# Kernel optimization log

Measured on AMD Instinct MI355X. Metric: run time of the kernel, lower is better.

Reference implementation:

```python
import jax, jax.numpy as jnp
import numpy as np

DIM = 1024
HEADS = 16
HEAD_DIM = DIM // HEADS
HIDDEN = 4 * DIM
B, N = 4, 2048


def _layernorm(x, g, b, eps=1e-5):
    mu = jnp.mean(x, axis=-1, keepdims=True)
    var = jnp.var(x, axis=-1, keepdims=True)
    return (x - mu) * jax.lax.rsqrt(var + eps) * g + b


def setup_inputs() -> dict:
    key = jax.random.key(0)
    ks = jax.random.split(key, 8)
    s_in = 1.0 / np.sqrt(DIM)
    s_hid = 1.0 / np.sqrt(HIDDEN)
    return {
        "x": jax.random.normal(ks[0], (B, N, DIM), jnp.float32),
        "w_qkv": jax.random.normal(ks[1], (DIM, 3 * DIM), jnp.float32) * s_in,
        "w_proj": jax.random.normal(ks[2], (DIM, DIM), jnp.float32) * s_in,
        "b_proj": jnp.zeros((DIM,), jnp.float32),
        "ln1_g": jnp.ones((DIM,), jnp.float32),
        "ln1_b": jnp.zeros((DIM,), jnp.float32),
        "w1": jax.random.normal(ks[3], (DIM, HIDDEN), jnp.float32) * s_in,
        "b1": jnp.zeros((HIDDEN,), jnp.float32),
        "w2": jax.random.normal(ks[4], (HIDDEN, DIM), jnp.float32) * s_hid,
        "b2": jnp.zeros((DIM,), jnp.float32),
        "ln2_g": jnp.ones((DIM,), jnp.float32),
        "ln2_b": jnp.zeros((DIM,), jnp.float32),
    }


def reference(x, w_qkv, w_proj, b_proj, ln1_g, ln1_b, w1, b1, w2, b2, ln2_g, ln2_b):
    # --- multi-head self-attention (pre-norm), dropout=0 (eval) ---
    h = _layernorm(x, ln1_g, ln1_b)
    qkv = h @ w_qkv                       # [B,N,3*DIM]
    qkv = qkv.reshape(B, N, 3, HEADS, HEAD_DIM)
    q = jnp.transpose(qkv[:, :, 0], (0, 2, 1, 3))  # [B,H,N,hd]
    k = jnp.transpose(qkv[:, :, 1], (0, 2, 1, 3))
    v = jnp.transpose(qkv[:, :, 2], (0, 2, 1, 3))
    scale = HEAD_DIM ** -0.5
    attn = jnp.einsum('bhqd,bhkd->bhqk', q, k) * scale  # [B,H,N,N]
    attn = jax.nn.softmax(attn, axis=-1)
    o = jnp.einsum('bhqk,bhkd->bhqd', attn, v)
    o = jnp.transpose(o, (0, 2, 1, 3)).reshape(B, N, DIM)
    x = o @ w_proj + b_proj + x
    # --- feed-forward (pre-norm), exact GELU ---
    h = _layernorm(x, ln2_g, ln2_b)
    h = jax.nn.gelu(h @ w1 + b1, approximate=False)
    return h @ w2 + b2 + x
```

## Files before the change

kernel.cpp:

```cpp
#include <hip/hip_runtime.h>
#include <cstdint>
#include <cstddef>

typedef float  v4f  __attribute__((ext_vector_type(4)));
typedef __bf16 v8bf __attribute__((ext_vector_type(8)));
typedef __bf16 v4bf __attribute__((ext_vector_type(4)));

__device__ __forceinline__ float b2f(unsigned short u) {
  union { unsigned int i; float f; } cv; cv.i = ((unsigned int)u) << 16; return cv.f;
}
__device__ __forceinline__ unsigned short f2b(float f) {
  union { float f; unsigned int i; } cv; cv.f = f;
  unsigned int i = cv.i;
  i += 0x7fffu + ((i >> 16) & 1u);
  return (unsigned short)(i >> 16);
}
__device__ __forceinline__ unsigned short f2b_trunc(float f) {
  union { float f; unsigned int i; } cv; cv.f = f;
  return (unsigned short)(cv.i >> 16);
}
__device__ __forceinline__ float gelu_fast(float x) {
  const float u = x * (1.5957691216f + 0.07135481627f * x * x);
  return x * (1.0f / (1.0f + __expf(-u)));
}
__device__ __forceinline__ void g2l16(const unsigned short* g, unsigned short* l) {
  __builtin_amdgcn_global_load_lds(
      (const __attribute__((address_space(1))) void*)g,
      (__attribute__((address_space(3))) void*)l,
      16, 0, 0);
}

__global__ __launch_bounds__(256) void transpose_k(const float* __restrict__ in,
                                                   unsigned short* __restrict__ out,
                                                   int R, int C) {
  __shared__ float tile[32][33];
  const int tx = threadIdx.x, ty = threadIdx.y;
  const int r0 = blockIdx.y * 32, c0 = blockIdx.x * 32;
#pragma unroll
  for (int j = 0; j < 4; ++j)
    tile[ty + 8 * j][tx] = in[(size_t)(r0 + ty + 8 * j) * C + c0 + tx];
  __syncthreads();
#pragma unroll
  for (int j = 0; j < 4; ++j)
    out[(size_t)(c0 + ty + 8 * j) * R + r0 + tx] = f2b(tile[tx][ty + 8 * j]);
}

__global__ __launch_bounds__(256) void ln_kernel(const void* __restrict__ xp, int in_bf16,
                                                 const float* __restrict__ g,
                                                 const float* __restrict__ bta,
                                                 unsigned short* __restrict__ out) {
  const int r = blockIdx.x, t = threadIdx.x;
  float v0, v1, v2, v3;
  if (in_bf16) {
    const ushort4 raw = *(const ushort4*)((const unsigned short*)xp + (size_t)r * 1024 + t * 4);
    v0 = b2f(raw.x); v1 = b2f(raw.y); v2 = b2f(raw.z); v3 = b2f(raw.w);
  } else {
    const float4 raw = *(const float4*)((const float*)xp + (size_t)r * 1024 + t * 4);
    v0 = raw.x; v1 = raw.y; v2 = raw.z; v3 = raw.w;
  }
  float s  = v0 + v1 + v2 + v3;
  float s2 = v0 * v0 + v1 * v1 + v2 * v2 + v3 * v3;
#pragma unroll
  for (int off = 32; off > 0; off >>= 1) {
    s  += __shfl_down(s, off);
    s2 += __shfl_down(s2, off);
  }
  __shared__ float red[8];
  const int w = t >> 6, lane = t & 63;
  if (lane == 0) { red[w] = s; red[4 + w] = s2; }
  __syncthreads();
  if (t == 0) {
    float ts = red[0] + red[1] + red[2] + red[3];
    float t2 = red[4] + red[5] + red[6] + red[7];
    float mu = ts * (1.0f / 1024.0f);
    float var = t2 * (1.0f / 1024.0f) - mu * mu;
    red[0] = mu;
    red[1] = rsqrtf(var + 1e-5f);
  }
  __syncthreads();
  const float mu = red[0], rs = red[1];
  const float4 graw = *(const float4*)(g + t * 4);
  const float4 braw = *(const float4*)(bta + t * 4);
  ushort4 o;
  o.x = f2b((v0 - mu) * rs * graw.x + braw.x);
  o.y = f2b((v1 - mu) * rs * graw.y + braw.y);
  o.z = f2b((v2 - mu) * rs * graw.z + braw.z);
  o.w = f2b((v3 - mu) * rs * graw.w + braw.w);
  *(ushort4*)(out + (size_t)r * 1024 + t * 4) = o;
}

__global__ __launch_bounds__(256, 2) void gemm_bt(const unsigned short* __restrict__ A,
                                                  const unsigned short* __restrict__ Bt,
                                                  const float* __restrict__ bias,
                                                  const void* __restrict__ res, int res_bf16,
                                                  void* __restrict__ Cout,
                                                  int M, int N, int K, int act, int out_bf16,
                                                  int swap_xy) {
  __shared__ __align__(16) unsigned short As[3][128 * 32];
  __shared__ __align__(16) unsigned short Bs[3][128 * 32];
  const int t = threadIdx.x;
  const int lane = t & 63, w = t >> 6;
  const int wr = (w >> 1) * 64, wc = (w & 1) * 64;
  const int lr = lane & 15, lq = lane >> 4;
  const int mb = swap_xy ? blockIdx.x : blockIdx.y;
  const int nb = swap_xy ? blockIdx.y : blockIdx.x;
  const int m0 = mb * 128, n0 = nb * 128;

  const int c0 = t, c1 = t + 256;
  const int r0 = c0 >> 2, o0 = (c0 & 3) << 3;
  const int r1 = c1 >> 2, o1 = (c1 & 3) << 3;
  const unsigned short* Ag0 = A  + (size_t)(m0 + r0) * K + o0;
  const unsigned short* Ag1 = A  + (size_t)(m0 + r1) * K + o1;
  const unsigned short* Bg0 = Bt + (size_t)(n0 + r0) * K + o0;
  const unsigned short* Bg1 = Bt + (size_t)(n0 + r1) * K + o1;

  v4f acc[4][4];
#pragma unroll
  for (int mi = 0; mi < 4; ++mi)
#pragma unroll
    for (int ni = 0; ni < 4; ++ni)
      acc[mi][ni] = (v4f){0.f, 0.f, 0.f, 0.f};

  const int nt = K >> 5;
  g2l16(Ag0, &As[0][c0 * 8]); g2l16(Bg0, &Bs[0][c0 * 8]);
  g2l16(Ag1, &As[0][c1 * 8]); g2l16(Bg1, &Bs[0][c1 * 8]);
  if (nt > 1) {
    g2l16(Ag0 + 32, &As[1][c0 * 8]); g2l16(Bg0 + 32, &Bs[1][c0 * 8]);
    g2l16(Ag1 + 32, &As[1][c1 * 8]); g2l16(Bg1 + 32, &Bs[1][c1 * 8]);
  }

  int bi = 0;
  for (int tt = 0; tt < nt; ++tt) {
    const int pf = tt + 2;
    if (pf < nt) {
      const int ko = pf << 5;
      const int pb = pf % 3;
      g2l16(Ag0 + ko, &As[pb][c0 * 8]); g2l16(Bg0 + ko, &Bs[pb][c0 * 8]);
      g2l16(Ag1 + ko, &As[pb][c1 * 8]); g2l16(Bg1 + ko, &Bs[pb][c1 * 8]);
      asm volatile("s_waitcnt vmcnt(8)" ::: "memory");
    } else if (tt + 1 < nt) {
      asm volatile("s_waitcnt vmcnt(4)" ::: "memory");
    } else {
      asm volatile("s_waitcnt vmcnt(0)" ::: "memory");
    }
    __builtin_amdgcn_s_barrier();
    asm volatile("" ::: "memory");

    v8bf af[4], bfr[4];
#pragma unroll
    for (int i = 0; i < 4; ++i) {
      af[i]  = *(const v8bf*)(&As[bi][(wr + i * 16 + lr) * 32 + lq * 8]);
      bfr[i] = *(const v8bf*)(&Bs[bi][(wc + i * 16 + lr) * 32 + lq * 8]);
    }
#pragma unroll
    for (int mi = 0; mi < 4; ++mi)
#pragma unroll
      for (int ni = 0; ni < 4; ++ni)
        acc[mi][ni] = __builtin_amdgcn_mfma_f32_16x16x32_bf16(af[mi], bfr[ni], acc[mi][ni], 0, 0, 0);

    asm volatile("" ::: "memory");
    __builtin_amdgcn_s_barrier();
    bi = (bi == 2) ? 0 : bi + 1;
  }

#pragma unroll
  for (int mi = 0; mi < 4; ++mi) {
#pragma unroll
    for (int ni = 0; ni < 4; ++ni) {
      const int col = n0 + wc + ni * 16 + lr;
      const float bv = bias ? bias[col] : 0.0f;
#pragma unroll
      for (int r = 0; r < 4; ++r) {
        const int row = m0 + wr + mi * 16 + lq * 4 + r;
        float v = acc[mi][ni][r] + bv;
        if (act) v = gelu_fast(v);
        if (res) {
          v += res_bf16 ? b2f(((const unsigned short*)res)[(size_t)row * N + col])
                        : ((const float*)res)[(size_t)row * N + col];
        }
        if (out_bf16)
          ((unsigned short*)Cout)[(size_t)row * N + col] = f2b(v);
        else
          ((float*)Cout)[(size_t)row * N + col] = v;
      }
    }
  }
}

__global__ __launch_bounds__(256) void vt_k(const unsigned short* __restrict__ qkv,
                                            unsigned short* __restrict__ Vt) {
  const int t = threadIdx.x;
  const int n = blockIdx.x * 256 + t, h = blockIdx.y, b = blockIdx.z;
  const size_t src = (size_t)(b * 2048 + n) * 3072 + 2048 + h * 64;
  unsigned short v[64];
#pragma unroll
  for (int j = 0; j < 8; ++j)
    *(uint4*)(v + j * 8) = *(const uint4*)(qkv + src + j * 8);
  const size_t dstbase = ((size_t)(b * 16 + h) * 64) * 2048 + n;
#pragma unroll
  for (int d = 0; d < 64; ++d)
    Vt[dstbase + (size_t)d * 2048] = v[d];
}

__global__ __launch_bounds__(256, 2) void attn_mfma(const unsigned short* __restrict__ qkv,
                                                    const unsigned short* __restrict__ Vt,
                                                    unsigned short* __restrict__ out) {
  __shared__ __align__(16) unsigned short Ks[64 * 80];
  __shared__ __align__(16) unsigned short Vs[64 * 80];
  __shared__ __align__(16) unsigned short Ps[4][32 * 76];
  const int t = threadIdx.x;
  const int lane = t & 63, w = t >> 6;
  const int lr = lane & 15, lq = lane >> 4;
  const int h = blockIdx.x, b = blockIdx.z;
  const int q0 = blockIdx.y * 128 + w * 32;

  v8bf aq[2][2];
#pragma unroll
  for (int mi = 0; mi < 2; ++mi)
#pragma unroll
    for (int kq = 0; kq < 2; ++kq)
      aq[mi][kq] = *(const v8bf*)(qkv + (size_t)(b * 2048 + q0 + mi * 16 + lr) * 3072
                                  + h * 64 + kq * 32 + lq * 8);

  v4f acc_o[2][4];
  float lsum[2][4];
#pragma unroll
  for (int mi = 0; mi < 2; ++mi)
#pragma unroll
    for (int di = 0; di < 4; ++di)
      acc_o[mi][di] = (v4f){0.f, 0.f, 0.f, 0.f};
#pragma unroll
  for (int mi = 0; mi < 2; ++mi)
#pragma unroll
    for (int r = 0; r < 4; ++r)
      lsum[mi][r] = 0.0f;

  const int sc0 = t, sc1 = t + 256;
  const int kr0 = sc0 >> 3, ko0 = (sc0 & 7) * 8;
  const int kr1 = sc1 >> 3, ko1 = (sc1 & 7) * 8;
  const unsigned short* Kg0 = qkv + (size_t)(b * 2048 + kr0) * 3072 + 1024 + h * 64 + ko0;
  const unsigned short* Kg1 = qkv + (size_t)(b * 2048 + kr1) * 3072 + 1024 + h * 64 + ko1;
  const unsigned short* Vg0 = Vt + ((size_t)(b * 16 + h) * 64 + kr0) * 2048 + ko0;
  const unsigned short* Vg1 = Vt + ((size_t)(b * 16 + h) * 64 + kr1) * 2048 + ko1;

  uint4 kreg0 = *(const uint4*)(Kg0);
  uint4 kreg1 = *(const uint4*)(Kg1);
  uint4 vreg0 = *(const uint4*)(Vg0);
  uint4 vreg1 = *(const uint4*)(Vg1);
  *(uint4*)(Ks + kr0 * 80 + ko0) = kreg0;
  *(uint4*)(Ks + kr1 * 80 + ko1) = kreg1;
  *(uint4*)(Vs + kr0 * 80 + ko0) = vreg0;
  *(uint4*)(Vs + kr1 * 80 + ko1) = vreg1;
  __syncthreads();

  for (int kt = 0; kt < 32; ++kt) {
    if (kt < 31) {
      const size_t kn = (size_t)(kt + 1) * 64;
      kreg0 = *(const uint4*)(Kg0 + kn * 3072);
      kreg1 = *(const uint4*)(Kg1 + kn * 3072);
      vreg0 = *(const uint4*)(Vg0 + kn);
      vreg1 = *(const uint4*)(Vg1 + kn);
    }

    v4f s_acc[2][4];
#pragma unroll
    for (int mi = 0; mi < 2; ++mi)
#pragma unroll
      for (int ni = 0; ni < 4; ++ni)
        s_acc[mi][ni] = (v4f){0.f, 0.f, 0.f, 0.f};
#pragma unroll
    for (int kq = 0; kq < 2; ++kq) {
      v8bf bk[4];
#pragma unroll
      for (int ni = 0; ni < 4; ++ni)
        bk[ni] = *(const v8bf*)(Ks + (ni * 16 + lr) * 80 + kq * 32 + lq * 8);
      __builtin_amdgcn_s_setprio(1);
#pragma unroll
      for (int mi = 0; mi < 2; ++mi)
#pragma unroll
        for (int ni = 0; ni < 4; ++ni)
          s_acc[mi][ni] = __builtin_amdgcn_mfma_f32_16x16x32_bf16(aq[mi][kq], bk[ni], s_acc[mi][ni], 0, 0, 0);
      __builtin_amdgcn_s_setprio(0);
    }

#pragma unroll
    for (int mi = 0; mi < 2; ++mi)
#pragma unroll
      for (int ni = 0; ni < 4; ++ni)
#pragma unroll
        for (int r = 0; r < 4; ++r) {
          const float p = __expf(s_acc[mi][ni][r] * 0.125f);
          const unsigned short pb = f2b_trunc(p);
          lsum[mi][r] += b2f(pb);
          Ps[w][(mi * 16 + lq * 4 + r) * 76 + ni * 16 + lr] = pb;
        }

#pragma unroll
    for (int ks = 0; ks < 2; ++ks) {
      v8bf ap[2], bv[4];
#pragma unroll
      for (int mi = 0; mi < 2; ++mi) {
        const unsigned short* base = Ps[w] + (mi * 16 + lr) * 76 + ks * 32 + lq * 8;
        const v4bf lo = *(const v4bf*)(base);
        const v4bf hi = *(const v4bf*)(base + 4);
        ap[mi] = __builtin_shufflevector(lo, hi, 0, 1, 2, 3, 4, 5, 6, 7);
      }
#pragma unroll
      for (int di = 0; di < 4; ++di)
        bv[di] = *(const v8bf*)(Vs + (di * 16 + lr) * 80 + ks * 32 + lq * 8);
      __builtin_amdgcn_s_setprio(1);
#pragma unroll
      for (int mi = 0; mi < 2; ++mi)
#pragma unroll
        for (int di = 0; di < 4; ++di)
          acc_o[mi][di] = __builtin_amdgcn_mfma_f32_16x16x32_bf16(ap[mi], bv[di], acc_o[mi][di], 0, 0, 0);
      __builtin_amdgcn_s_setprio(0);
    }

    __syncthreads();
    if (kt < 31) {
      *(uint4*)(Ks + kr0 * 80 + ko0) = kreg0;
      *(uint4*)(Ks + kr1 * 80 + ko1) = kreg1;
      *(uint4*)(Vs + kr0 * 80 + ko0) = vreg0;
      *(uint4*)(Vs + kr1 * 80 + ko1) = vreg1;
    }
    __syncthreads();
  }

#pragma unroll
  for (int mi = 0; mi < 2; ++mi)
#pragma unroll
    for (int r = 0; r < 4; ++r) {
      float v = lsum[mi][r];
      v += __shfl_xor(v, 1);
      v += __shfl_xor(v, 2);
      v += __shfl_xor(v, 4);
      v += __shfl_xor(v, 8);
      lsum[mi][r] = 1.0f / v;
    }

#pragma unroll
  for (int mi = 0; mi < 2; ++mi)
#pragma unroll
    for (int di = 0; di < 4; ++di)
#pragma unroll
      for (int r = 0; r < 4; ++r)
        out[(size_t)(b * 2048 + q0 + mi * 16 + lq * 4 + r) * 1024 + h * 64 + di * 16 + lr] =
            f2b(acc_o[mi][di][r] * lsum[mi][r]);
}

extern "C" void kernel_launch(void* const* d_in, const int* in_sizes, int n_in,
                              void* d_out, int out_size, void* d_ws, size_t ws_size,
                              hipStream_t stream) {
  (void)in_sizes; (void)n_in; (void)out_size; (void)ws_size;
  const float* x      = (const float*)d_in[0];
  const float* w_qkv  = (const float*)d_in[1];
  const float* w_proj = (const float*)d_in[2];
  const float* b_proj = (const float*)d_in[3];
  const float* ln1_g  = (const float*)d_in[4];
  const float* ln1_b  = (const float*)d_in[5];
  const float* w1     = (const float*)d_in[6];
  const float* b1     = (const float*)d_in[7];
  const float* w2     = (const float*)d_in[8];
  const float* b2     = (const float*)d_in[9];
  const float* ln2_g  = (const float*)d_in[10];
  const float* ln2_b  = (const float*)d_in[11];
  float* out = (float*)d_out;

  char* ws = (char*)d_ws;
  unsigned short* T_a   = (unsigned short*)(ws);
  unsigned short* T_b   = (unsigned short*)(ws + 8388608);
  unsigned short* x2buf = (unsigned short*)(ws + 16777216);
  unsigned short* Vtbuf = (unsigned short*)(ws + 33554432);
  unsigned short* Hbuf  = (unsigned short*)(ws + 50331648);
  unsigned short* qkvb  = (unsigned short*)(ws + 67108864);
  unsigned short* h3buf = (unsigned short*)(ws + 50331648);
  unsigned short* h2buf = (unsigned short*)d_out;

  const dim3 tb(32, 8);
  transpose_k<<<dim3(96, 32),  tb, 0, stream>>>(w_qkv,  T_a, 1024, 3072);
  transpose_k<<<dim3(32, 32),  tb, 0, stream>>>(w_proj, T_b, 1024, 1024);
  ln_kernel<<<8192, 256, 0, stream>>>(x, 0, ln1_g, ln1_b, Hbuf);
  gemm_bt<<<dim3(24, 64), 256, 0, stream>>>(Hbuf, T_a, nullptr, nullptr, 0, qkvb, 8192, 3072, 1024, 0, 1, 0);
  transpose_k<<<dim3(128, 32), tb, 0, stream>>>(w1, T_a, 1024, 4096);
  vt_k<<<dim3(8, 16, 4), 256, 0, stream>>>(qkvb, Vtbuf);
  attn_mfma<<<dim3(16, 16, 4), 256, 0, stream>>>(qkvb, Vtbuf, Hbuf);
  gemm_bt<<<dim3(64, 8), 256, 0, stream>>>(Hbuf, T_b, b_proj, x, 0, x2buf, 8192, 1024, 1024, 0, 1, 1);
  transpose_k<<<dim3(32, 128), tb, 0, stream>>>(w2, T_b, 4096, 1024);
  ln_kernel<<<8192, 256, 0, stream>>>(x2buf, 1, ln2_g, ln2_b, h2buf);
  gemm_bt<<<dim3(32, 64), 256, 0, stream>>>(h2buf, T_a, b1, nullptr, 0, h3buf, 8192, 4096, 1024, 1, 1, 0);
  gemm_bt<<<dim3(64, 8), 256, 0, stream>>>(h3buf, T_b, b2, x2buf, 1, out, 8192, 1024, 4096, 0, 0, 1);
}
```

Baseline: 583.7 us.

## Swizzle GEMM LDS layout and load attention K/V directly from global

The GEMM kernel now XOR-swizzles the column chunk used for global-to-LDS staging, and the MFMA fragment reads use the matching swizzled offset. This is meant to reduce LDS bank conflicts. The attention kernel drops its shared K/V tiles and block-wide barriers: each wave reads its K and V fragments straight from global memory (relying on cache reuse across waves), and the occupancy hint is raised to 4 blocks. This removes synchronization and LDS traffic, but every wave now issues redundant global loads and no longer prefetches the next tile, so it may expose memory latency.

```diff
diff --git a/kernel.cpp b/kernel.cpp
--- a/kernel.cpp
+++ b/kernel.cpp
@@ -107,12 +107,14 @@
   const int m0 = mb * 128, n0 = nb * 128;
 
   const int c0 = t, c1 = t + 256;
-  const int r0 = c0 >> 2, o0 = (c0 & 3) << 3;
-  const int r1 = c1 >> 2, o1 = (c1 & 3) << 3;
+  const int r0 = c0 >> 2, o0 = (((c0 & 3) ^ ((c0 >> 3) & 3)) << 3);
+  const int r1 = c1 >> 2, o1 = (((c1 & 3) ^ ((c1 >> 3) & 3)) << 3);
   const unsigned short* Ag0 = A  + (size_t)(m0 + r0) * K + o0;
   const unsigned short* Ag1 = A  + (size_t)(m0 + r1) * K + o1;
   const unsigned short* Bg0 = Bt + (size_t)(n0 + r0) * K + o0;
   const unsigned short* Bg1 = Bt + (size_t)(n0 + r1) * K + o1;
+
+  const int ra = ((lq ^ ((lr >> 1) & 3)) << 3);
 
   v4f acc[4][4];
 #pragma unroll
@@ -149,8 +151,8 @@
     v8bf af[4], bfr[4];
 #pragma unroll
     for (int i = 0; i < 4; ++i) {
-      af[i]  = *(const v8bf*)(&As[bi][(wr + i * 16 + lr) * 32 + lq * 8]);
-      bfr[i] = *(const v8bf*)(&Bs[bi][(wc + i * 16 + lr) * 32 + lq * 8]);
+      af[i]  = *(const v8bf*)(&As[bi][(wr + i * 16 + lr) * 32 + ra]);
+      bfr[i] = *(const v8bf*)(&Bs[bi][(wc + i * 16 + lr) * 32 + ra]);
     }
 #pragma unroll
     for (int mi = 0; mi < 4; ++mi)
@@ -202,11 +204,9 @@
     Vt[dstbase + (size_t)d * 2048] = v[d];
 }
 
-__global__ __launch_bounds__(256, 2) void attn_mfma(const unsigned short* __restrict__ qkv,
+__global__ __launch_bounds__(256, 4) void attn_mfma(const unsigned short* __restrict__ qkv,
                                                     const unsigned short* __restrict__ Vt,
                                                     unsigned short* __restrict__ out) {
-  __shared__ __align__(16) unsigned short Ks[64 * 80];
-  __shared__ __align__(16) unsigned short Vs[64 * 80];
   __shared__ __align__(16) unsigned short Ps[4][32 * 76];
   const int t = threadIdx.x;
   const int lane = t & 63, w = t >> 6;
@@ -235,32 +235,11 @@
     for (int r = 0; r < 4; ++r)
       lsum[mi][r] = 0.0f;
 
-  const int sc0 = t, sc1 = t + 256;
-  const int kr0 = sc0 >> 3, ko0 = (sc0 & 7) * 8;
-  const int kr1 = sc1 >> 3, ko1 = (sc1 & 7) * 8;
-  const unsigned short* Kg0 = qkv + (size_t)(b * 2048 + kr0) * 3072 + 1024 + h * 64 + ko0;
-  const unsigned short* Kg1 = qkv + (size_t)(b * 2048 + kr1) * 3072 + 1024 + h * 64 + ko1;
-  const unsigned short* Vg0 = Vt + ((size_t)(b * 16 + h) * 64 + kr0) * 2048 + ko0;
-  const unsigned short* Vg1 = Vt + ((size_t)(b * 16 + h) * 64 + kr1) * 2048 + ko1;
-
-  uint4 kreg0 = *(const uint4*)(Kg0);
-  uint4 kreg1 = *(const uint4*)(Kg1);
-  uint4 vreg0 = *(const uint4*)(Vg0);
-  uint4 vreg1 = *(const uint4*)(Vg1);
-  *(uint4*)(Ks + kr0 * 80 + ko0) = kreg0;
-  *(uint4*)(Ks + kr1 * 80 + ko1) = kreg1;
-  *(uint4*)(Vs + kr0 * 80 + ko0) = vreg0;
-  *(uint4*)(Vs + kr1 * 80 + ko1) = vreg1;
-  __syncthreads();
+  const unsigned short* Kb = qkv + (size_t)b * 2048 * 3072 + 1024 + h * 64 + lq * 8;
+  const unsigned short* Vb = Vt + ((size_t)(b * 16 + h) * 64 + lr) * 2048 + lq * 8;
 
   for (int kt = 0; kt < 32; ++kt) {
-    if (kt < 31) {
-      const size_t kn = (size_t)(kt + 1) * 64;
-      kreg0 = *(const uint4*)(Kg0 + kn * 3072);
-      kreg1 = *(const uint4*)(Kg1 + kn * 3072);
-      vreg0 = *(const uint4*)(Vg0 + kn);
-      vreg1 = *(const uint4*)(Vg1 + kn);
-    }
+    const int kt0 = kt * 64;
 
     v4f s_acc[2][4];
 #pragma unroll
@@ -273,7 +252,7 @@
       v8bf bk[4];
 #pragma unroll
       for (int ni = 0; ni < 4; ++ni)
-        bk[ni] = *(const v8bf*)(Ks + (ni * 16 + lr) * 80 + kq * 32 + lq * 8);
+        bk[ni] = *(const v8bf*)(Kb + (size_t)(kt0 + ni * 16 + lr) * 3072 + kq * 32);
       __builtin_amdgcn_s_setprio(1);
 #pragma unroll
       for (int mi = 0; mi < 2; ++mi)
@@ -282,6 +261,13 @@
           s_acc[mi][ni] = __builtin_amdgcn_mfma_f32_16x16x32_bf16(aq[mi][kq], bk[ni], s_acc[mi][ni], 0, 0, 0);
       __builtin_amdgcn_s_setprio(0);
     }
+
+    v8bf bv[2][4];
+#pragma unroll
+    for (int ks = 0; ks < 2; ++ks)
+#pragma unroll
+      for (int di = 0; di < 4; ++di)
+        bv[ks][di] = *(const v8bf*)(Vb + (size_t)(di * 16) * 2048 + kt0 + ks * 32);
 
 #pragma unroll
     for (int mi = 0; mi < 2; ++mi)
@@ -297,7 +283,7 @@
 
 #pragma unroll
     for (int ks = 0; ks < 2; ++ks) {
-      v8bf ap[2], bv[4];
+      v8bf ap[2];
 #pragma unroll
       for (int mi = 0; mi < 2; ++mi) {
         const unsigned short* base = Ps[w] + (mi * 16 + lr) * 76 + ks * 32 + lq * 8;
@@ -305,26 +291,14 @@
         const v4bf hi = *(const v4bf*)(base + 4);
         ap[mi] = __builtin_shufflevector(lo, hi, 0, 1, 2, 3, 4, 5, 6, 7);
       }
-#pragma unroll
-      for (int di = 0; di < 4; ++di)
-        bv[di] = *(const v8bf*)(Vs + (di * 16 + lr) * 80 + ks * 32 + lq * 8);
       __builtin_amdgcn_s_setprio(1);
 #pragma unroll
       for (int mi = 0; mi < 2; ++mi)
 #pragma unroll
         for (int di = 0; di < 4; ++di)
-          acc_o[mi][di] = __builtin_amdgcn_mfma_f32_16x16x32_bf16(ap[mi], bv[di], acc_o[mi][di], 0, 0, 0);
+          acc_o[mi][di] = __builtin_amdgcn_mfma_f32_16x16x32_bf16(ap[mi], bv[ks][di], acc_o[mi][di], 0, 0, 0);
       __builtin_amdgcn_s_setprio(0);
     }
-
-    __syncthreads();
-    if (kt < 31) {
-      *(uint4*)(Ks + kr0 * 80 + ko0) = kreg0;
-      *(uint4*)(Ks + kr1 * 80 + ko1) = kreg1;
-      *(uint4*)(Vs + kr0 * 80 + ko0) = vreg0;
-      *(uint4*)(Vs + kr1 * 80 + ko1) = vreg1;
-    }
-    __syncthreads();
   }
 
 #pragma unroll
```

Result: slower. 751.8 us (+28.8%).

## Enlarge GEMM tile to 256x128 with XOR-swizzled LDS layout

Applied to the files above, without the earlier changes.

The GEMM block tile grows from 128x128 to 256x128, with each wave computing a 128x64 output (8x4 MFMA tiles), and all GEMM launch grids are halved in M to match. The LDS chunk offsets are XOR-swizzled on both the global-to-LDS store and the fragment reads to reduce bank conflicts. This raises arithmetic intensity per B-tile load and cuts the number of blocks. In exchange it doubles the accumulator registers and uses more LDS (about 72 KB), which may lower occupancy below the launch bound. It also leaves fewer blocks for the N=1024 GEMMs (256 blocks).

```diff
diff --git a/kernel.cpp b/kernel.cpp
--- a/kernel.cpp
+++ b/kernel.cpp
@@ -96,75 +96,91 @@
                                                   void* __restrict__ Cout,
                                                   int M, int N, int K, int act, int out_bf16,
                                                   int swap_xy) {
-  __shared__ __align__(16) unsigned short As[3][128 * 32];
+  __shared__ __align__(16) unsigned short As[3][256 * 32];
   __shared__ __align__(16) unsigned short Bs[3][128 * 32];
   const int t = threadIdx.x;
   const int lane = t & 63, w = t >> 6;
-  const int wr = (w >> 1) * 64, wc = (w & 1) * 64;
+  const int wr = (w >> 1) * 128, wc = (w & 1) * 64;
   const int lr = lane & 15, lq = lane >> 4;
   const int mb = swap_xy ? blockIdx.x : blockIdx.y;
   const int nb = swap_xy ? blockIdx.y : blockIdx.x;
-  const int m0 = mb * 128, n0 = nb * 128;
-
-  const int c0 = t, c1 = t + 256;
-  const int r0 = c0 >> 2, o0 = (c0 & 3) << 3;
-  const int r1 = c1 >> 2, o1 = (c1 & 3) << 3;
-  const unsigned short* Ag0 = A  + (size_t)(m0 + r0) * K + o0;
-  const unsigned short* Ag1 = A  + (size_t)(m0 + r1) * K + o1;
-  const unsigned short* Bg0 = Bt + (size_t)(n0 + r0) * K + o0;
-  const unsigned short* Bg1 = Bt + (size_t)(n0 + r1) * K + o1;
-
-  v4f acc[4][4];
-#pragma unroll
-  for (int mi = 0; mi < 4; ++mi)
+  const int m0 = mb * 256, n0 = nb * 128;
+
+  const unsigned short* Ag0;
+  const unsigned short* Ag1;
+  const unsigned short* Ag2;
+  const unsigned short* Ag3;
+  const unsigned short* Bg0;
+  const unsigned short* Bg1;
+  {
+    const int cA0 = t,        rA0 = cA0 >> 2, oA0 = (((cA0 & 3) ^ ((cA0 >> 3) & 3)) << 3);
+    const int cA1 = t + 256,  rA1 = cA1 >> 2, oA1 = (((cA1 & 3) ^ ((cA1 >> 3) & 3)) << 3);
+    const int cA2 = t + 512,  rA2 = cA2 >> 2, oA2 = (((cA2 & 3) ^ ((cA2 >> 3) & 3)) << 3);
+    const int cA3 = t + 768,  rA3 = cA3 >> 2, oA3 = (((cA3 & 3) ^ ((cA3 >> 3) & 3)) << 3);
+    Ag0 = A + (size_t)(m0 + rA0) * K + oA0;
+    Ag1 = A + (size_t)(m0 + rA1) * K + oA1;
+    Ag2 = A + (size_t)(m0 + rA2) * K + oA2;
+    Ag3 = A + (size_t)(m0 + rA3) * K + oA3;
+    Bg0 = Bt + (size_t)(n0 + rA0) * K + oA0;
+    Bg1 = Bt + (size_t)(n0 + rA1) * K + oA1;
+  }
+  const int ra = ((lq ^ ((lr >> 1) & 3)) << 3);
+
+  v4f acc[8][4];
+#pragma unroll
+  for (int mi = 0; mi < 8; ++mi)
 #pragma unroll
     for (int ni = 0; ni < 4; ++ni)
       acc[mi][ni] = (v4f){0.f, 0.f, 0.f, 0.f};
 
+#define STAGE(buf, ko)                                  \
+  do {                                                  \
+    g2l16(Ag0 + (ko), &As[buf][(t)*8]);                 \
+    g2l16(Ag1 + (ko), &As[buf][(t + 256) * 8]);         \
+    g2l16(Ag2 + (ko), &As[buf][(t + 512) * 8]);         \
+    g2l16(Ag3 + (ko), &As[buf][(t + 768) * 8]);         \
+    g2l16(Bg0 + (ko), &Bs[buf][(t)*8]);                 \
+    g2l16(Bg1 + (ko), &Bs[buf][(t + 256) * 8]);         \
+  } while (0)
+
   const int nt = K >> 5;
-  g2l16(Ag0, &As[0][c0 * 8]); g2l16(Bg0, &Bs[0][c0 * 8]);
-  g2l16(Ag1, &As[0][c1 * 8]); g2l16(Bg1, &Bs[0][c1 * 8]);
-  if (nt > 1) {
-    g2l16(Ag0 + 32, &As[1][c0 * 8]); g2l16(Bg0 + 32, &Bs[1][c0 * 8]);
-    g2l16(Ag1 + 32, &As[1][c1 * 8]); g2l16(Bg1 + 32, &Bs[1][c1 * 8]);
-  }
+  STAGE(0, 0);
+  STAGE(1, 32);
 
   int bi = 0;
   for (int tt = 0; tt < nt; ++tt) {
     const int pf = tt + 2;
     if (pf < nt) {
-      const int ko = pf << 5;
-      const int pb = pf % 3;
-      g2l16(Ag0 + ko, &As[pb][c0 * 8]); g2l16(Bg0 + ko, &Bs[pb][c0 * 8]);
-      g2l16(Ag1 + ko, &As[pb][c1 * 8]); g2l16(Bg1 + ko, &Bs[pb][c1 * 8]);
-      asm volatile("s_waitcnt vmcnt(8)" ::: "memory");
+      STAGE(pf % 3, pf << 5);
+      asm volatile("s_waitcnt vmcnt(12)" ::: "memory");
     } else if (tt + 1 < nt) {
-      asm volatile("s_waitcnt vmcnt(4)" ::: "memory");
+      asm volatile("s_waitcnt vmcnt(6)" ::: "memory");
     } else {
       asm volatile("s_waitcnt vmcnt(0)" ::: "memory");
     }
     __builtin_amdgcn_s_barrier();
     asm volatile("" ::: "memory");
 
-    v8bf af[4], bfr[4];
-#pragma unroll
-    for (int i = 0; i < 4; ++i) {
-      af[i]  = *(const v8bf*)(&As[bi][(wr + i * 16 + lr) * 32 + lq * 8]);
-      bfr[i] = *(const v8bf*)(&Bs[bi][(wc + i * 16 + lr) * 32 + lq * 8]);
-    }
-#pragma unroll
-    for (int mi = 0; mi < 4; ++mi)
+    v8bf bfr[4];
+#pragma unroll
+    for (int i = 0; i < 4; ++i)
+      bfr[i] = *(const v8bf*)(&Bs[bi][(wc + i * 16 + lr) * 32 + ra]);
+#pragma unroll
+    for (int mi = 0; mi < 8; ++mi) {
+      const v8bf af = *(const v8bf*)(&As[bi][(wr + mi * 16 + lr) * 32 + ra]);
 #pragma unroll
       for (int ni = 0; ni < 4; ++ni)
-        acc[mi][ni] = __builtin_amdgcn_mfma_f32_16x16x32_bf16(af[mi], bfr[ni], acc[mi][ni], 0, 0, 0);
+        acc[mi][ni] = __builtin_amdgcn_mfma_f32_16x16x32_bf16(af, bfr[ni], acc[mi][ni], 0, 0, 0);
+    }
 
     asm volatile("" ::: "memory");
     __builtin_amdgcn_s_barrier();
     bi = (bi == 2) ? 0 : bi + 1;
   }
-
-#pragma unroll
-  for (int mi = 0; mi < 4; ++mi) {
+#undef STAGE
+
+#pragma unroll
+  for (int mi = 0; mi < 8; ++mi) {
 #pragma unroll
     for (int ni = 0; ni < 4; ++ni) {
       const int col = n0 + wc + ni * 16 + lr;
@@ -313,7 +329,7 @@
       for (int mi = 0; mi < 2; ++mi)
 #pragma unroll
         for (int di = 0; di < 4; ++di)
-          acc_o[mi][di] = __builtin_amdgcn_mfma_f32_16x16x32_bf16(ap[mi], bv[di], acc_o[mi][di], 0, 0, 0);
+          acc_o[mi][di] = __builtin_amdgcn_mfma_f32_16x16x32_bf16(ap[mi], bv[ks == 0 ? di : di], acc_o[mi][di], 0, 0, 0);
       __builtin_amdgcn_s_setprio(0);
     }
 
@@ -381,13 +397,13 @@
   transpose_k<<<dim3(96, 32),  tb, 0, stream>>>(w_qkv,  T_a, 1024, 3072);
   transpose_k<<<dim3(32, 32),  tb, 0, stream>>>(w_proj, T_b, 1024, 1024);
   ln_kernel<<<8192, 256, 0, stream>>>(x, 0, ln1_g, ln1_b, Hbuf);
-  gemm_bt<<<dim3(24, 64), 256, 0, stream>>>(Hbuf, T_a, nullptr, nullptr, 0, qkvb, 8192, 3072, 1024, 0, 1, 0);
+  gemm_bt<<<dim3(24, 32), 256, 0, stream>>>(Hbuf, T_a, nullptr, nullptr, 0, qkvb, 8192, 3072, 1024, 0, 1, 0);
   transpose_k<<<dim3(128, 32), tb, 0, stream>>>(w1, T_a, 1024, 4096);
   vt_k<<<dim3(8, 16, 4), 256, 0, stream>>>(qkvb, Vtbuf);
   attn_mfma<<<dim3(16, 16, 4), 256, 0, stream>>>(qkvb, Vtbuf, Hbuf);
-  gemm_bt<<<dim3(64, 8), 256, 0, stream>>>(Hbuf, T_b, b_proj, x, 0, x2buf, 8192, 1024, 1024, 0, 1, 1);
+  gemm_bt<<<dim3(32, 8), 256, 0, stream>>>(Hbuf, T_b, b_proj, x, 0, x2buf, 8192, 1024, 1024, 0, 1, 1);
   transpose_k<<<dim3(32, 128), tb, 0, stream>>>(w2, T_b, 4096, 1024);
   ln_kernel<<<8192, 256, 0, stream>>>(x2buf, 1, ln2_g, ln2_b, h2buf);
-  gemm_bt<<<dim3(32, 64), 256, 0, stream>>>(h2buf, T_a, b1, nullptr, 0, h3buf, 8192, 4096, 1024, 1, 1, 0);
-  gemm_bt<<<dim3(64, 8), 256, 0, stream>>>(h3buf, T_b, b2, x2buf, 1, out, 8192, 1024, 4096, 0, 0, 1);
-}
+  gemm_bt<<<dim3(32, 32), 256, 0, stream>>>(h2buf, T_a, b1, nullptr, 0, h3buf, 8192, 4096, 1024, 1, 1, 0);
+  gemm_bt<<<dim3(32, 8), 256, 0, stream>>>(h3buf, T_b, b2, x2buf, 1, out, 8192, 1024, 4096, 0, 0, 1);
+}
```

After: 672.4 us. 1.15x slower.

## Replace GEMM with 8-wave 256xBN tile kernel using swizzled LDS and phased MFMA

Applied to the files above, without the earlier changes.

Replaces the 128x128 four-wave GEMM with a templated eight-wave kernel that uses 256x256 or 256x128 output tiles, a K-step of 64, and double-buffered LDS. The LDS layout gets an XOR swizzle to avoid bank conflicts. The MFMA work is split into quadrant phases, with barriers and s_setprio, so the A and B stage-ins are interleaved with compute. The goal is more data reuse per block and better overlap of global loads with MFMA. In exchange it uses more registers and LDS per block, and fewer blocks on the projection and FFN2 GEMMs (256 blocks) may leave CUs underfilled.

```diff
diff --git a/kernel.cpp b/kernel.cpp
--- a/kernel.cpp
+++ b/kernel.cpp
@@ -89,84 +89,177 @@
   *(ushort4*)(out + (size_t)r * 1024 + t * 4) = o;
 }
 
-__global__ __launch_bounds__(256, 2) void gemm_bt(const unsigned short* __restrict__ A,
-                                                  const unsigned short* __restrict__ Bt,
-                                                  const float* __restrict__ bias,
-                                                  const void* __restrict__ res, int res_bf16,
-                                                  void* __restrict__ Cout,
-                                                  int M, int N, int K, int act, int out_bf16,
-                                                  int swap_xy) {
-  __shared__ __align__(16) unsigned short As[3][128 * 32];
-  __shared__ __align__(16) unsigned short Bs[3][128 * 32];
+template <int NREP>
+__global__ __launch_bounds__(512, 2) void gemm8p(const unsigned short* __restrict__ A,
+                                                 const unsigned short* __restrict__ Bt,
+                                                 const float* __restrict__ bias,
+                                                 const void* __restrict__ res, int res_bf16,
+                                                 void* __restrict__ Cout,
+                                                 int M, int N, int K, int act, int out_bf16,
+                                                 int swap_xy) {
+  constexpr int BN = NREP * 64;
+  __shared__ __align__(16) unsigned short As[2][256 * 64];
+  __shared__ __align__(16) unsigned short Bs[2][BN * 64];
   const int t = threadIdx.x;
-  const int lane = t & 63, w = t >> 6;
-  const int wr = (w >> 1) * 64, wc = (w & 1) * 64;
+  const int lane = t & 63;
   const int lr = lane & 15, lq = lane >> 4;
+  const int wid = t >> 6;
+  const int wm = wid >> 2, wn = wid & 3;
   const int mb = swap_xy ? blockIdx.x : blockIdx.y;
   const int nb = swap_xy ? blockIdx.y : blockIdx.x;
-  const int m0 = mb * 128, n0 = nb * 128;
-
-  const int c0 = t, c1 = t + 256;
-  const int r0 = c0 >> 2, o0 = (c0 & 3) << 3;
-  const int r1 = c1 >> 2, o1 = (c1 & 3) << 3;
-  const unsigned short* Ag0 = A  + (size_t)(m0 + r0) * K + o0;
-  const unsigned short* Ag1 = A  + (size_t)(m0 + r1) * K + o1;
-  const unsigned short* Bg0 = Bt + (size_t)(n0 + r0) * K + o0;
-  const unsigned short* Bg1 = Bt + (size_t)(n0 + r1) * K + o1;
-
-  v4f acc[4][4];
-#pragma unroll
-  for (int mi = 0; mi < 4; ++mi)
-#pragma unroll
-    for (int ni = 0; ni < 4; ++ni)
+  const int m0 = mb * 256, n0 = nb * BN;
+
+  const int srow = t >> 3;
+  const int schunk = (t & 7) ^ (srow & 7);
+  const unsigned short* Agp[4];
+  const unsigned short* Bgp[NREP];
+#pragma unroll
+  for (int j = 0; j < 4; ++j)
+    Agp[j] = A + (size_t)(m0 + j * 64 + srow) * K + schunk * 8;
+#pragma unroll
+  for (int j = 0; j < NREP; ++j)
+    Bgp[j] = Bt + (size_t)(n0 + j * 64 + srow) * K + schunk * 8;
+
+  auto stageA = [&](int dbuf, int ko) {
+#pragma unroll
+    for (int j = 0; j < 4; ++j)
+      g2l16(Agp[j] + ko, &As[dbuf][j * 4096 + t * 8]);
+  };
+  auto stageB = [&](int dbuf, int ko) {
+#pragma unroll
+    for (int j = 0; j < NREP; ++j)
+      g2l16(Bgp[j] + ko, &Bs[dbuf][j * 4096 + t * 8]);
+  };
+  auto lda = [&](int dbuf, int mi, int kq) -> v8bf {
+    return *(const v8bf*)(&As[dbuf][(wm * 128 + mi * 16 + lr) * 64 +
+                                    (((kq * 4 + lq) ^ (lr & 7)) << 3)]);
+  };
+  auto ldb = [&](int dbuf, int ni, int kq) -> v8bf {
+    return *(const v8bf*)(&Bs[dbuf][(wn * (BN / 4) + ni * 16 + lr) * 64 +
+                                    (((kq * 4 + lq) ^ (lr & 7)) << 3)]);
+  };
+
+  v4f acc[8][NREP];
+#pragma unroll
+  for (int mi = 0; mi < 8; ++mi)
+#pragma unroll
+    for (int ni = 0; ni < NREP; ++ni)
       acc[mi][ni] = (v4f){0.f, 0.f, 0.f, 0.f};
 
-  const int nt = K >> 5;
-  g2l16(Ag0, &As[0][c0 * 8]); g2l16(Bg0, &Bs[0][c0 * 8]);
-  g2l16(Ag1, &As[0][c1 * 8]); g2l16(Bg1, &Bs[0][c1 * 8]);
-  if (nt > 1) {
-    g2l16(Ag0 + 32, &As[1][c0 * 8]); g2l16(Bg0 + 32, &Bs[1][c0 * 8]);
-    g2l16(Ag1 + 32, &As[1][c1 * 8]); g2l16(Bg1 + 32, &Bs[1][c1 * 8]);
-  }
-
-  int bi = 0;
-  for (int tt = 0; tt < nt; ++tt) {
-    const int pf = tt + 2;
-    if (pf < nt) {
-      const int ko = pf << 5;
-      const int pb = pf % 3;
-      g2l16(Ag0 + ko, &As[pb][c0 * 8]); g2l16(Bg0 + ko, &Bs[pb][c0 * 8]);
-      g2l16(Ag1 + ko, &As[pb][c1 * 8]); g2l16(Bg1 + ko, &Bs[pb][c1 * 8]);
-      asm volatile("s_waitcnt vmcnt(8)" ::: "memory");
-    } else if (tt + 1 < nt) {
-      asm volatile("s_waitcnt vmcnt(4)" ::: "memory");
+  const int NT = K >> 6;
+  stageA(0, 0);
+  stageB(0, 0);
+
+  for (int kt = 0; kt < NT; ++kt) {
+    const int buf = kt & 1, nbuf = buf ^ 1;
+    const bool pre = (kt + 1) < NT;
+    const int ko = (kt + 1) << 6;
+
+    if constexpr (NREP == 4) {
+      v8bf aL[4][2], aH[4][2], bL[2][2], bH[2][2];
+      if (pre) {
+        stageA(nbuf, ko);
+        asm volatile("s_waitcnt vmcnt(4)" ::: "memory");
+      } else {
+        asm volatile("s_waitcnt vmcnt(0)" ::: "memory");
+      }
+      __builtin_amdgcn_s_barrier();
+#pragma unroll
+      for (int mi = 0; mi < 4; ++mi) { aL[mi][0] = lda(buf, mi, 0); aL[mi][1] = lda(buf, mi, 1); }
+#pragma unroll
+      for (int ni = 0; ni < 2; ++ni) { bL[ni][0] = ldb(buf, ni, 0); bL[ni][1] = ldb(buf, ni, 1); }
+      __builtin_amdgcn_s_setprio(1);
+#pragma unroll
+      for (int mi = 0; mi < 4; ++mi)
+#pragma unroll
+        for (int ni = 0; ni < 2; ++ni)
+#pragma unroll
+          for (int kq = 0; kq < 2; ++kq)
+            acc[mi][ni] = __builtin_amdgcn_mfma_f32_16x16x32_bf16(aL[mi][kq], bL[ni][kq], acc[mi][ni], 0, 0, 0);
+      __builtin_amdgcn_s_setprio(0);
+      __builtin_amdgcn_s_barrier();
+#pragma unroll
+      for (int ni = 0; ni < 2; ++ni) { bH[ni][0] = ldb(buf, ni + 2, 0); bH[ni][1] = ldb(buf, ni + 2, 1); }
+      if (pre) stageB(nbuf, ko);
+      __builtin_amdgcn_s_barrier();
+      __builtin_amdgcn_s_setprio(1);
+#pragma unroll
+      for (int mi = 0; mi < 4; ++mi)
+#pragma unroll
+        for (int ni = 0; ni < 2; ++ni)
+#pragma unroll
+          for (int kq = 0; kq < 2; ++kq)
+            acc[mi][ni + 2] = __builtin_amdgcn_mfma_f32_16x16x32_bf16(aL[mi][kq], bH[ni][kq], acc[mi][ni + 2], 0, 0, 0);
+      __builtin_amdgcn_s_setprio(0);
+      __builtin_amdgcn_s_barrier();
+#pragma unroll
+      for (int mi = 0; mi < 4; ++mi) { aH[mi][0] = lda(buf, mi + 4, 0); aH[mi][1] = lda(buf, mi + 4, 1); }
+      __builtin_amdgcn_s_barrier();
+      __builtin_amdgcn_s_setprio(1);
+#pragma unroll
+      for (int mi = 0; mi < 4; ++mi)
+#pragma unroll
+        for (int ni = 0; ni < 2; ++ni)
+#pragma unroll
+          for (int kq = 0; kq < 2; ++kq)
+            acc[mi + 4][ni] = __builtin_amdgcn_mfma_f32_16x16x32_bf16(aH[mi][kq], bL[ni][kq], acc[mi + 4][ni], 0, 0, 0);
+      __builtin_amdgcn_s_setprio(0);
+      __builtin_amdgcn_s_barrier();
+      __builtin_amdgcn_s_setprio(1);
+#pragma unroll
+      for (int mi = 0; mi < 4; ++mi)
+#pragma unroll
+        for (int ni = 0; ni < 2; ++ni)
+#pragma unroll
+          for (int kq = 0; kq < 2; ++kq)
+            acc[mi + 4][ni + 2] = __builtin_amdgcn_mfma_f32_16x16x32_bf16(aH[mi][kq], bH[ni][kq], acc[mi + 4][ni + 2], 0, 0, 0);
+      __builtin_amdgcn_s_setprio(0);
+      __builtin_amdgcn_s_barrier();
     } else {
-      asm volatile("s_waitcnt vmcnt(0)" ::: "memory");
-    }
-    __builtin_amdgcn_s_barrier();
-    asm volatile("" ::: "memory");
-
-    v8bf af[4], bfr[4];
-#pragma unroll
-    for (int i = 0; i < 4; ++i) {
-      af[i]  = *(const v8bf*)(&As[bi][(wr + i * 16 + lr) * 32 + lq * 8]);
-      bfr[i] = *(const v8bf*)(&Bs[bi][(wc + i * 16 + lr) * 32 + lq * 8]);
-    }
-#pragma unroll
-    for (int mi = 0; mi < 4; ++mi)
-#pragma unroll
-      for (int ni = 0; ni < 4; ++ni)
-        acc[mi][ni] = __builtin_amdgcn_mfma_f32_16x16x32_bf16(af[mi], bfr[ni], acc[mi][ni], 0, 0, 0);
-
-    asm volatile("" ::: "memory");
-    __builtin_amdgcn_s_barrier();
-    bi = (bi == 2) ? 0 : bi + 1;
-  }
-
-#pragma unroll
-  for (int mi = 0; mi < 4; ++mi) {
-#pragma unroll
-    for (int ni = 0; ni < 4; ++ni) {
+      v8bf aL[4][2], aH[4][2], bb[2][2];
+      if (pre) {
+        stageA(nbuf, ko);
+        asm volatile("s_waitcnt vmcnt(4)" ::: "memory");
+      } else {
+        asm volatile("s_waitcnt vmcnt(0)" ::: "memory");
+      }
+      __builtin_amdgcn_s_barrier();
+#pragma unroll
+      for (int mi = 0; mi < 4; ++mi) { aL[mi][0] = lda(buf, mi, 0); aL[mi][1] = lda(buf, mi, 1); }
+#pragma unroll
+      for (int ni = 0; ni < 2; ++ni) { bb[ni][0] = ldb(buf, ni, 0); bb[ni][1] = ldb(buf, ni, 1); }
+      __builtin_amdgcn_s_setprio(1);
+#pragma unroll
+      for (int mi = 0; mi < 4; ++mi)
+#pragma unroll
+        for (int ni = 0; ni < 2; ++ni)
+#pragma unroll
+          for (int kq = 0; kq < 2; ++kq)
+            acc[mi][ni] = __builtin_amdgcn_mfma_f32_16x16x32_bf16(aL[mi][kq], bb[ni][kq], acc[mi][ni], 0, 0, 0);
+      __builtin_amdgcn_s_setprio(0);
+      __builtin_amdgcn_s_barrier();
+#pragma unroll
+      for (int mi = 0; mi < 4; ++mi) { aH[mi][0] = lda(buf, mi + 4, 0); aH[mi][1] = lda(buf, mi + 4, 1); }
+      if (pre) stageB(nbuf, ko);
+      __builtin_amdgcn_s_barrier();
+      __builtin_amdgcn_s_setprio(1);
+#pragma unroll
+      for (int mi = 0; mi < 4; ++mi)
+#pragma unroll
+        for (int ni = 0; ni < 2; ++ni)
+#pragma unroll
+          for (int kq = 0; kq < 2; ++kq)
+            acc[mi + 4][ni] = __builtin_amdgcn_mfma_f32_16x16x32_bf16(aH[mi][kq], bb[ni][kq], acc[mi + 4][ni], 0, 0, 0);
+      __builtin_amdgcn_s_setprio(0);
+      __builtin_amdgcn_s_barrier();
+    }
+  }
+
+  const int wr = wm * 128, wc = wn * (BN / 4);
+#pragma unroll
+  for (int mi = 0; mi < 8; ++mi) {
+#pragma unroll
+    for (int ni = 0; ni < NREP; ++ni) {
       const int col = n0 + wc + ni * 16 + lr;
       const float bv = bias ? bias[col] : 0.0f;
 #pragma unroll
@@ -381,13 +474,13 @@
   transpose_k<<<dim3(96, 32),  tb, 0, stream>>>(w_qkv,  T_a, 1024, 3072);
   transpose_k<<<dim3(32, 32),  tb, 0, stream>>>(w_proj, T_b, 1024, 1024);
   ln_kernel<<<8192, 256, 0, stream>>>(x, 0, ln1_g, ln1_b, Hbuf);
-  gemm_bt<<<dim3(24, 64), 256, 0, stream>>>(Hbuf, T_a, nullptr, nullptr, 0, qkvb, 8192, 3072, 1024, 0, 1, 0);
+  gemm8p<4><<<dim3(12, 32), 512, 0, stream>>>(Hbuf, T_a, nullptr, nullptr, 0, qkvb, 8192, 3072, 1024, 0, 1, 0);
   transpose_k<<<dim3(128, 32), tb, 0, stream>>>(w1, T_a, 1024, 4096);
   vt_k<<<dim3(8, 16, 4), 256, 0, stream>>>(qkvb, Vtbuf);
   attn_mfma<<<dim3(16, 16, 4), 256, 0, stream>>>(qkvb, Vtbuf, Hbuf);
-  gemm_bt<<<dim3(64, 8), 256, 0, stream>>>(Hbuf, T_b, b_proj, x, 0, x2buf, 8192, 1024, 1024, 0, 1, 1);
+  gemm8p<2><<<dim3(32, 8), 512, 0, stream>>>(Hbuf, T_b, b_proj, x, 0, x2buf, 8192, 1024, 1024, 0, 1, 1);
   transpose_k<<<dim3(32, 128), tb, 0, stream>>>(w2, T_b, 4096, 1024);
   ln_kernel<<<8192, 256, 0, stream>>>(x2buf, 1, ln2_g, ln2_b, h2buf);
-  gemm_bt<<<dim3(32, 64), 256, 0, stream>>>(h2buf, T_a, b1, nullptr, 0, h3buf, 8192, 4096, 1024, 1, 1, 0);
-  gemm_bt<<<dim3(64, 8), 256, 0, stream>>>(h3buf, T_b, b2, x2buf, 1, out, 8192, 1024, 4096, 0, 0, 1);
-}
+  gemm8p<4><<<dim3(16, 32), 512, 0, stream>>>(h2buf, T_a, b1, nullptr, 0, h3buf, 8192, 4096, 1024, 1, 1, 0);
+  gemm8p<2><<<dim3(32, 8), 512, 0, stream>>>(h3buf, T_b, b2, x2buf, 1, out, 8192, 1024, 4096, 0, 0, 1);
+}
```

New measurement: 617.0 us. +5.7%, slower.
